# Performance work log

Hardware: AMD Instinct MI355X
Metric: run time of the kernel (lower is better)

Reference implementation:

```python
import jax, jax.numpy as jnp
import numpy as np

B, QLEN, KLEN = 4, 512, 1024
KDIM = QDIM = ADIM = 512
H_MA, H_CA = 4, 2
CHUNK = 4
EPS = 1e-6
SHARP = 1.0
SCALE = float(np.sqrt(ADIM))


def moving_sum(x, back, forward):
    # moving sum over last axis with window [i-back, i+forward] (matches F.conv1d with ones filter)
    nb = [(0, 0)] * (x.ndim - 1)
    cs = jnp.cumsum(jnp.pad(x, nb + [(back, forward)]), axis=-1)
    cs = jnp.pad(cs, nb + [(1, 0)])
    w = back + forward + 1
    return cs[..., w:] - cs[..., :-w]


def setup_inputs() -> dict:
    key = jax.random.key(0)
    ks = jax.random.split(key, 16)
    s = 0.02
    f32 = jnp.float32
    return {
        'key_t': jax.random.normal(ks[0], (B, KLEN, KDIM), f32),
        'query': jax.random.normal(ks[1], (B, QLEN, QDIM), f32),
        # monotonic energy params
        'wk_ma': jax.random.normal(ks[2], (KDIM, ADIM), f32) * s,
        'bk_ma': jnp.zeros((ADIM,), f32),
        'wq_ma': jax.random.normal(ks[3], (QDIM, ADIM), f32) * s,
        'bq_ma': jnp.zeros((ADIM,), f32),
        'r': jnp.array([-4.0], f32),
        # chunk energy params
        'wk_ca': jax.random.normal(ks[4], (KDIM, ADIM), f32) * s,
        'bk_ca': jnp.zeros((ADIM,), f32),
        'wq_ca': jax.random.normal(ks[5], (QDIM, ADIM), f32) * s,
        'bq_ca': jnp.zeros((ADIM,), f32),
        # value / output projections
        'wv': jax.random.normal(ks[6], (KDIM, ADIM), f32) * s,
        'bv': jnp.zeros((ADIM,), f32),
        'wo': jax.random.normal(ks[7], (ADIM, ADIM), f32) * s,
        'bo': jnp.zeros((ADIM,), f32),
    }


def reference(key_t, query, wk_ma, bk_ma, wq_ma, bq_ma, r,
              wk_ca, bk_ca, wq_ca, bq_ca, wv, bv, wo, bo):
    # ---- monotonic energy (scaled_dot) -> [B, H_ma, qlen, klen]
    dk = ADIM // H_MA
    k_ma = (key_t @ wk_ma + bk_ma).reshape(B, KLEN, H_MA, dk).transpose(0, 2, 1, 3)
    q_ma = (query @ wq_ma + bq_ma).reshape(B, QLEN, H_MA, dk).transpose(0, 2, 1, 3)
    e_ma = jnp.einsum('bhqd,bhkd->bhqk', q_ma, k_ma) / SCALE + r[0]

    # ---- selection probabilities + safe cumprod of (1 - p) (exclusive, in log space)
    p = jax.nn.sigmoid(e_ma)                              # [B,H,q,k]
    log1mp = jnp.log(jnp.clip(1.0 - p, EPS, 1.0))
    cp = jnp.exp(jnp.cumsum(log1mp, axis=-1) - log1mp)    # exclusive cumprod

    # ---- monotonic alignment alpha via recurrence over query steps (parallel MoChA)
    aw0 = jnp.zeros((B, H_MA, KLEN), p.dtype).at[:, :, 0].set(1.0)

    def step(aw_prev, pc):
        p_i, cp_i = pc  # [B,H,k]
        a = p_i * cp_i * jnp.cumsum(aw_prev / jnp.clip(cp_i, EPS, 1.0), axis=-1)
        return a, a

    _, alpha_q = jax.lax.scan(step, aw0, (jnp.moveaxis(p, 2, 0), jnp.moveaxis(cp, 2, 0)))
    alpha = jnp.moveaxis(alpha_q, 0, 2)                   # [B,H_ma,q,k]

    # ---- chunk energy (scaled_dot, shared across MA heads) -> [B, H_ca, qlen, klen]
    dkc = ADIM // H_CA
    k_ca = (key_t @ wk_ca + bk_ca).reshape(B, KLEN, H_CA, dkc).transpose(0, 2, 1, 3)
    q_ca = (query @ wq_ca + bq_ca).reshape(B, QLEN, H_CA, dkc).transpose(0, 2, 1, 3)
    e_ca = jnp.einsum('bhqd,bhkd->bhqk', q_ca, k_ca) / SCALE

    # ---- efficient chunkwise attention: clipped-exp softmax within moving window
    u = e_ca - jnp.max(e_ca, axis=-1, keepdims=True)
    se = jnp.maximum(jnp.exp(u), 1e-5)                    # [B,H_ca,q,k]
    denom = moving_sum(se, CHUNK - 1, 0)                  # [B,H_ca,q,k]
    frac = alpha[:, :, None] * SHARP / denom[:, None]     # [B,H_ma,H_ca,q,k]
    beta = se[:, None] * moving_sum(frac, 0, CHUNK - 1)   # [B,H_ma,H_ca,q,k]
    beta = beta.reshape(B, H_MA * H_CA, QLEN, KLEN)

    # ---- context vector and output projection
    h = H_MA * H_CA
    dv = ADIM // h
    v = (key_t @ wv + bv).reshape(B, KLEN, h, dv).transpose(0, 2, 1, 3)
    cv = jnp.einsum('bhqk,bhkd->bhqd', beta, v)
    cv = cv.transpose(0, 2, 1, 3).reshape(B, QLEN, ADIM)
    return cv @ wo + bo
```

## Files before the change

kernel.cpp:

```cpp
#include <hip/hip_runtime.h>
#include <hip/hip_bf16.h>
#include <math.h>

#define DEV_INLINE __device__ __forceinline__

typedef float f32x4 __attribute__((ext_vector_type(4)));
typedef short bf16x8 __attribute__((ext_vector_type(8)));
typedef short s16x4 __attribute__((ext_vector_type(4)));

constexpr int B_    = 4;
constexpr int QLEN  = 512;
constexpr int KLEN  = 1024;
constexpr int DIM   = 512;
constexpr int H_MA  = 4;
constexpr int H_CA  = 2;
constexpr int CHUNK = 4;
constexpr float EPS = 1e-6f;
constexpr float INV_SCALE = 1.0f / 22.62741699796952f;


DEV_INLINE unsigned short f2bf(float x) {
    unsigned int u = __float_as_uint(x);
    unsigned int r = u + 0x7FFFu + ((u >> 16) & 1u);
    return (unsigned short)(r >> 16);
}

DEV_INLINE void split2(float x, short& h, short& l) {
    const unsigned short hb = f2bf(x);
    const float hf = __uint_as_float(((unsigned int)hb) << 16);
    h = (short)hb;
    l = (short)f2bf(x - hf);
}

DEV_INLINE float bf2f(short s) {
    return __uint_as_float(((unsigned int)(unsigned short)s) << 16);
}

__global__ __launch_bounds__(256) void rowsplit2_kernel(
    const float* __restrict__ X0, short* __restrict__ H0, short* __restrict__ L0, int n0_4,
    const float* __restrict__ X1, short* __restrict__ H1, short* __restrict__ L1, int n1_4)
{
    int i = blockIdx.x * 256 + threadIdx.x;
    const float* X; short* Xh; short* Xl;
    if (i < n0_4) { X = X0; Xh = H0; Xl = L0; }
    else {
        i -= n0_4;
        if (i >= n1_4) return;
        X = X1; Xh = H1; Xl = L1;
    }
    const f32x4 v = *(const f32x4*)(X + (size_t)i * 4);
    s16x4 h, l;
#pragma unroll
    for (int j = 0; j < 4; ++j) {
        short hh, ll;
        split2(v[j], hh, ll);
        h[j] = hh; l[j] = ll;
    }
    *(s16x4*)(Xh + (size_t)i * 4) = h;
    *(s16x4*)(Xl + (size_t)i * 4) = l;
}

__global__ __launch_bounds__(256) void transsplit6_kernel(
    const float* __restrict__ w0, const float* __restrict__ w1,
    const float* __restrict__ w2, const float* __restrict__ w3,
    const float* __restrict__ w4, const float* __restrict__ w5,
    short* __restrict__ WTkh, short* __restrict__ WTkl,
    short* __restrict__ WTqh, short* __restrict__ WTql,
    short* __restrict__ WToh, short* __restrict__ WTol)
{
    const float* W; short* Dh; short* Dl;
    const int zz = blockIdx.z;
    const int MS = 512 * 512;
    switch (zz) {
        case 0: W = w0; Dh = WTkh;          Dl = WTkl;          break;
        case 1: W = w1; Dh = WTkh + MS;     Dl = WTkl + MS;     break;
        case 2: W = w2; Dh = WTkh + 2 * MS; Dl = WTkl + 2 * MS; break;
        case 3: W = w3; Dh = WTqh;          Dl = WTql;          break;
        case 4: W = w4; Dh = WTqh + MS;     Dl = WTql + MS;     break;
        default: W = w5; Dh = WToh;         Dl = WTol;          break;
    }

    __shared__ __align__(16) short Th[64][72];
    __shared__ __align__(16) short Tl[64][72];
    const int t = threadIdx.x;
    const int k0 = blockIdx.x * 64;
    const int n0 = blockIdx.y * 64;
#pragma unroll
    for (int i = 0; i < 4; ++i) {
        const int c  = t + 256 * i;
        const int kr = c >> 4;
        const int nc = c & 15;
        const f32x4 v = *(const f32x4*)(W + (size_t)(k0 + kr) * DIM + n0 + nc * 4);
#pragma unroll
        for (int j = 0; j < 4; ++j) {
            short h, l;
            split2(v[j], h, l);
            Th[nc * 4 + j][kr] = h;
            Tl[nc * 4 + j][kr] = l;
        }
    }
    __syncthreads();
#pragma unroll
    for (int i = 0; i < 4; ++i) {
        const int c  = t + 256 * i;
        const int nr = c >> 4;
        const int kc = c & 15;
        *(s16x4*)(Dh + (size_t)(n0 + nr) * DIM + k0 + kc * 4) = *(const s16x4*)&Th[nr][kc * 4];
        *(s16x4*)(Dl + (size_t)(n0 + nr) * DIM + k0 + kc * 4) = *(const s16x4*)&Tl[nr][kc * 4];
    }
}


DEV_INLINE void mfma128_nt_core(
    const short* __restrict__ Ah, const short* __restrict__ Al, int lda,
    const short* __restrict__ Bh, const short* __restrict__ Bl, int ldb,
    int K, int bm, int bn, f32x4 (&acc)[4][4])
{
    __shared__ __align__(16) short AsH[8][4][16][8];
    __shared__ __align__(16) short AsL[8][4][16][8];
    __shared__ __align__(16) short BsH[8][4][16][8];
    __shared__ __align__(16) short BsL[8][4][16][8];
    const int tid  = threadIdx.x;
    const int lane = tid & 63;
    const int w    = tid >> 6;
    const int wm   = w >> 1, wn = w & 1;
    const int lkg  = lane >> 4, lrow = lane & 15;

    for (int k0 = 0; k0 < K; k0 += 32) {
        bf16x8 vah[2], val[2], vbh[2], vbl[2];
#pragma unroll
        for (int p = 0; p < 2; ++p) {
            const int c = p * 256 + tid;
            const int row = c >> 2, kk = c & 3;
            const size_t ao = (size_t)(bm + row) * lda + k0 + kk * 8;
            const size_t bo = (size_t)(bn + row) * ldb + k0 + kk * 8;
            vah[p] = *(const bf16x8*)(Ah + ao);
            val[p] = *(const bf16x8*)(Al + ao);
            vbh[p] = *(const bf16x8*)(Bh + bo);
            vbl[p] = *(const bf16x8*)(Bl + bo);
        }
        __syncthreads();
#pragma unroll
        for (int p = 0; p < 2; ++p) {
            const int c = p * 256 + tid;
            const int row = c >> 2, kk = c & 3;
            const int fm = row >> 4, rr = row & 15;
            *(bf16x8*)&AsH[fm][kk][rr][0] = vah[p];
            *(bf16x8*)&AsL[fm][kk][rr][0] = val[p];
            *(bf16x8*)&BsH[fm][kk][rr][0] = vbh[p];
            *(bf16x8*)&BsL[fm][kk][rr][0] = vbl[p];
        }
        __syncthreads();

        bf16x8 bhf[4], blf[4];
#pragma unroll
        for (int fn = 0; fn < 4; ++fn) {
            bhf[fn] = *(const bf16x8*)&BsH[wn * 4 + fn][lkg][lrow][0];
            blf[fn] = *(const bf16x8*)&BsL[wn * 4 + fn][lkg][lrow][0];
        }
#pragma unroll
        for (int fm = 0; fm < 4; ++fm) {
            const bf16x8 ah = *(const bf16x8*)&AsH[wm * 4 + fm][lkg][lrow][0];
            const bf16x8 al = *(const bf16x8*)&AsL[wm * 4 + fm][lkg][lrow][0];
#pragma unroll
            for (int fn = 0; fn < 4; ++fn) {
                acc[fm][fn] = __builtin_amdgcn_mfma_f32_16x16x32_bf16(ah, bhf[fn], acc[fm][fn], 0, 0, 0);
                acc[fm][fn] = __builtin_amdgcn_mfma_f32_16x16x32_bf16(ah, blf[fn], acc[fm][fn], 0, 0, 0);
                acc[fm][fn] = __builtin_amdgcn_mfma_f32_16x16x32_bf16(al, bhf[fn], acc[fm][fn], 0, 0, 0);
            }
        }
    }
}

__global__ __launch_bounds__(256) void proj_both_kernel(
    const short* __restrict__ Kh, const short* __restrict__ Kl,
    const short* __restrict__ Qh, const short* __restrict__ Ql,
    const short* __restrict__ WTkh, const short* __restrict__ WTkl,
    const short* __restrict__ WTqh, const short* __restrict__ WTql,
    short* __restrict__ KPh, short* __restrict__ KPl,
    short* __restrict__ QPh, short* __restrict__ QPl,
    const float* __restrict__ bkma, const float* __restrict__ bkca,
    const float* __restrict__ bvv_,
    const float* __restrict__ bqma, const float* __restrict__ bqca)
{
    const int bid = blockIdx.x;
    const short *Ah, *Al, *Bh, *Bl;
    short *Ch, *Cl;
    const float *b0, *b1, *b2;
    int bm, bn, ldc;
    if (bid < 384) {
        bm = (bid & 31) * 128; bn = (bid >> 5) * 128;
        Ah = Kh; Al = Kl; Bh = WTkh; Bl = WTkl;
        Ch = KPh; Cl = KPl; ldc = 1536;
        b0 = bkma; b1 = bkca; b2 = bvv_;
    } else {
        const int r = bid - 384;
        bm = (r & 15) * 128; bn = (r >> 4) * 128;
        Ah = Qh; Al = Ql; Bh = WTqh; Bl = WTql;
        Ch = QPh; Cl = QPl; ldc = 1024;
        b0 = bqma; b1 = bqca; b2 = bqca;
    }

    f32x4 acc[4][4] = {};
    mfma128_nt_core(Ah, Al, DIM, Bh, Bl, DIM, DIM, bm, bn, acc);
    const int lane = threadIdx.x & 63;
    const int w = threadIdx.x >> 6;
    const int wm = w >> 1, wn = w & 1;
#pragma unroll
    for (int fm = 0; fm < 4; ++fm)
#pragma unroll
        for (int fn = 0; fn < 4; ++fn) {
            const int col = bn + wn * 64 + fn * 16 + (lane & 15);
            const int seg = col >> 9, cs = col & 511;
            const float bvv = seg == 0 ? b0[cs] : (seg == 1 ? b1[cs] : b2[cs]);
#pragma unroll
            for (int j = 0; j < 4; ++j) {
                const int row = bm + wm * 64 + fm * 16 + (lane >> 4) * 4 + j;
                short h, l;
                split2(acc[fm][fn][j] + bvv, h, l);
                Ch[(size_t)row * ldc + col] = h;
                Cl[(size_t)row * ldc + col] = l;
            }
        }
}

__global__ __launch_bounds__(256) void energy_both_kernel(
    const short* __restrict__ QPh, const short* __restrict__ QPl,
    const short* __restrict__ KPh, const short* __restrict__ KPl,
    float* __restrict__ EMA, float* __restrict__ ECA,
    const float* __restrict__ radd)
{
    const int gz = blockIdx.z;
    int colA0, colB0, HD;
    float* E;
    float addv;
    int b, h;
    if (gz < 16) {
        b = gz >> 2; h = gz & 3;
        colA0 = 0; colB0 = 0; HD = 128;
        E = EMA + (size_t)gz * QLEN * KLEN;
        addv = radd[0];
    } else {
        const int z = gz - 16;
        b = z >> 1; h = z & 1;
        colA0 = 512; colB0 = 512; HD = 256;
        E = ECA + (size_t)z * QLEN * KLEN;
        addv = 0.0f;
    }
    const short* Ah = QPh + (size_t)b * QLEN * 1024 + colA0 + h * HD;
    const short* Al = QPl + (size_t)b * QLEN * 1024 + colA0 + h * HD;
    const short* Bh = KPh + (size_t)b * KLEN * 1536 + colB0 + h * HD;
    const short* Bl = KPl + (size_t)b * KLEN * 1536 + colB0 + h * HD;

    f32x4 acc[4][4] = {};
    const int bm = blockIdx.x * 128, bn = blockIdx.y * 128;
    mfma128_nt_core(Ah, Al, 1024, Bh, Bl, 1536, HD, bm, bn, acc);
    const int lane = threadIdx.x & 63;
    const int w = threadIdx.x >> 6;
    const int wm = w >> 1, wn = w & 1;
#pragma unroll
    for (int fm = 0; fm < 4; ++fm)
#pragma unroll
        for (int fn = 0; fn < 4; ++fn) {
            const int col = bn + wn * 64 + fn * 16 + (lane & 15);
#pragma unroll
            for (int j = 0; j < 4; ++j) {
                const int row = bm + wm * 64 + fm * 16 + (lane >> 4) * 4 + j;
                E[(size_t)row * KLEN + col] = acc[fm][fn][j] * INV_SCALE + addv;
            }
        }
}


DEV_INLINE void mfma_nt_core(const short* __restrict__ Ah, const short* __restrict__ Al, int lda,
                             const short* __restrict__ Bh, const short* __restrict__ Bl, int ldb,
                             int K, int bm, int bn, f32x4 (&acc)[2][2])
{
    __shared__ __align__(16) short AsH[4][4][16][8];
    __shared__ __align__(16) short AsL[4][4][16][8];
    __shared__ __align__(16) short BsH[4][4][16][8];
    __shared__ __align__(16) short BsL[4][4][16][8];
    const int tid  = threadIdx.x;
    const int lane = tid & 63;
    const int w    = tid >> 6;
    const int wm   = w >> 1, wn = w & 1;
    const int r    = tid >> 2;
    const int kg   = tid & 3;
    const int rb   = r >> 4, rr = r & 15;
    const int lkg  = lane >> 4, lrr = lane & 15;

    for (int k0 = 0; k0 < K; k0 += 32) {
        const bf16x8 avh = *(const bf16x8*)(Ah + (size_t)(bm + r) * lda + k0 + kg * 8);
        const bf16x8 avl = *(const bf16x8*)(Al + (size_t)(bm + r) * lda + k0 + kg * 8);
        const bf16x8 bvh = *(const bf16x8*)(Bh + (size_t)(bn + r) * ldb + k0 + kg * 8);
        const bf16x8 bvl = *(const bf16x8*)(Bl + (size_t)(bn + r) * ldb + k0 + kg * 8);
        __syncthreads();
        *(bf16x8*)&AsH[rb][kg][rr][0] = avh;
        *(bf16x8*)&AsL[rb][kg][rr][0] = avl;
        *(bf16x8*)&BsH[rb][kg][rr][0] = bvh;
        *(bf16x8*)&BsL[rb][kg][rr][0] = bvl;
        __syncthreads();
#pragma unroll
        for (int fm = 0; fm < 2; ++fm) {
            const bf16x8 ah = *(const bf16x8*)&AsH[wm * 2 + fm][lkg][lrr][0];
            const bf16x8 al = *(const bf16x8*)&AsL[wm * 2 + fm][lkg][lrr][0];
#pragma unroll
            for (int fn = 0; fn < 2; ++fn) {
                const bf16x8 bh = *(const bf16x8*)&BsH[wn * 2 + fn][lkg][lrr][0];
                const bf16x8 bl = *(const bf16x8*)&BsL[wn * 2 + fn][lkg][lrr][0];
                acc[fm][fn] = __builtin_amdgcn_mfma_f32_16x16x32_bf16(ah, bh, acc[fm][fn], 0, 0, 0);
                acc[fm][fn] = __builtin_amdgcn_mfma_f32_16x16x32_bf16(ah, bl, acc[fm][fn], 0, 0, 0);
                acc[fm][fn] = __builtin_amdgcn_mfma_f32_16x16x32_bf16(al, bh, acc[fm][fn], 0, 0, 0);
            }
        }
    }
}

__global__ __launch_bounds__(256) void mfma_nt_f32_kernel(
    const short* __restrict__ Ah, const short* __restrict__ Al, int lda,
    const short* __restrict__ Bh, const short* __restrict__ Bl, int ldb,
    float* __restrict__ C, int ldc, int K,
    const float* __restrict__ bias)
{
    f32x4 acc[2][2] = {};
    const int bm = blockIdx.x * 64, bn = blockIdx.y * 64;
    mfma_nt_core(Ah, Al, lda, Bh, Bl, ldb, K, bm, bn, acc);
    const int lane = threadIdx.x & 63;
    const int w = threadIdx.x >> 6;
    const int wm = w >> 1, wn = w & 1;
#pragma unroll
    for (int fm = 0; fm < 2; ++fm)
#pragma unroll
        for (int fn = 0; fn < 2; ++fn) {
            const int col = bn + wn * 32 + fn * 16 + (lane & 15);
            const float bvv = bias ? bias[col] : 0.0f;
#pragma unroll
            for (int j = 0; j < 4; ++j) {
                const int row = bm + wm * 32 + fm * 16 + (lane >> 4) * 4 + j;
                C[(size_t)row * ldc + col] = acc[fm][fn][j] + bvv;
            }
        }
}


__global__ __launch_bounds__(256) void rows_kernel(
    float* __restrict__ PCP, float* __restrict__ ICP,
    float* __restrict__ SE, float* __restrict__ RDEN)
{
    const int bid = blockIdx.x;
    const int tid = threadIdx.x;
    const int lane = tid & 63, wid = tid >> 6;

    if (bid < B_ * H_MA * QLEN) {
        const size_t row = bid;
        float* pe = PCP + row * KLEN;
        float* pi = ICP + row * KLEN;

        const float4 ev = *(const float4*)(pe + tid * 4);
        float e[4] = {ev.x, ev.y, ev.z, ev.w};
        float p[4], l[4], s[4];
        float run = 0.0f;
#pragma unroll
        for (int j = 0; j < 4; ++j) {
            p[j] = 1.0f / (1.0f + expf(-e[j]));
            float om = 1.0f - p[j];
            om = fminf(fmaxf(om, EPS), 1.0f);
            l[j] = logf(om);
            run += l[j];
            s[j] = run;
        }
        const float t = run;
        float v = t;
#pragma unroll
        for (int off = 1; off < 64; off <<= 1) {
            const float u = __shfl_up(v, off);
            if (lane >= off) v += u;
        }
        __shared__ float wsum[4];
        if (lane == 63) wsum[wid] = v;
        __syncthreads();
        float base = v - t;
        for (int w = 0; w < wid; ++w) base += wsum[w];

        float4 po, io;
        float* pp = (float*)&po;
        float* ip = (float*)&io;
#pragma unroll
        for (int j = 0; j < 4; ++j) {
            const float cum = base + s[j];
            const float cp  = expf(cum - l[j]);
            pp[j] = p[j] * cp;
            ip[j] = 1.0f / fmaxf(cp, EPS);
        }
        *(float4*)(pe + tid * 4) = po;
        *(float4*)(pi + tid * 4) = io;
    } else {
        const size_t row = bid - B_ * H_MA * QLEN;
        float* ps = SE + row * KLEN;
        float* pd = RDEN + row * KLEN;

        const float4 ev = *(const float4*)(ps + tid * 4);
        float e[4] = {ev.x, ev.y, ev.z, ev.w};
        float m = fmaxf(fmaxf(e[0], e[1]), fmaxf(e[2], e[3]));
#pragma unroll
        for (int off = 32; off >= 1; off >>= 1)
            m = fmaxf(m, __shfl_xor(m, off));
        __shared__ float wmax[4];
        if (lane == 0) wmax[wid] = m;
        __syncthreads();
        m = fmaxf(fmaxf(wmax[0], wmax[1]), fmaxf(wmax[2], wmax[3]));

        __shared__ float sh[KLEN + 3];
        if (tid < 3) sh[tid] = 0.0f;
        float se[4];
#pragma unroll
        for (int j = 0; j < 4; ++j) {
            se[j] = fmaxf(expf(e[j] - m), 1e-5f);
            sh[3 + tid * 4 + j] = se[j];
        }
        __syncthreads();
        float4 so, do_;
        float* sp = (float*)&so;
        float* dp = (float*)&do_;
#pragma unroll
        for (int j = 0; j < 4; ++j) {
            const int k = tid * 4 + j;
            sp[j] = se[j];
            dp[j] = 1.0f / (sh[3 + k] + sh[2 + k] + sh[1 + k] + sh[k]);
        }
        *(float4*)(ps + tid * 4) = so;
        *(float4*)(pd + tid * 4) = do_;
    }
}


template<int CTRL, int ROW_MASK>
DEV_INLINE float dpp_add(float x) {
    int t = __builtin_amdgcn_update_dpp(0, __float_as_int(x), CTRL, ROW_MASK, 0xf, true);
    return x + __int_as_float(t);
}

DEV_INLINE float wave64_incl_scan(float x) {
    x = dpp_add<0x111, 0xf>(x);
    x = dpp_add<0x112, 0xf>(x);
    x = dpp_add<0x114, 0xf>(x);
    x = dpp_add<0x118, 0xf>(x);
    x = dpp_add<0x142, 0xa>(x);
    x = dpp_add<0x143, 0xc>(x);
    return x;
}

typedef __attribute__((address_space(3))) void lv_t;
typedef __attribute__((address_space(1))) const void gv_t;

DEV_INLINE void dma16(const float* g, float* l) {
    __builtin_amdgcn_global_load_lds((gv_t*)g, (lv_t*)l, 16, 0, 0);
}

template<int N> DEV_INLINE void vwait() {
    asm volatile("s_waitcnt vmcnt(%0)" :: "i"(N) : "memory");
    __builtin_amdgcn_sched_barrier(0);
}

template<int N> DEV_INLINE void lwait() {
    asm volatile("s_waitcnt lgkmcnt(%0)" :: "i"(N));
    __builtin_amdgcn_sched_barrier(0);
}

DEV_INLINE void ldsr4(f32x4& d, const float* a_) {
    const unsigned off = (unsigned)(size_t)(lv_t*)a_;
    asm volatile("ds_read_b128 %0, %1" : "=v"(d) : "v"(off));
}

DEV_INLINE void dswr1(float* a_, float v) {
    const unsigned off = (unsigned)(size_t)(lv_t*)a_;
    asm volatile("ds_write_b32 %0, %1" :: "v"(off), "v"(v));
}

DEV_INLINE void sbar() {
    asm volatile("s_barrier" ::: "memory");
}

#define ASTEP(WAITN, BUF, NBUF, PAR, DO_READ, DO_DMA, CG, NG)         \
    {                                                                 \
        vwait<WAITN>();                                               \
        if (DO_READ) {                                                \
            ldsr4(p##NG, &ring[NBUF][0][qoff]);                       \
            ldsr4(i##NG, &ring[NBUF][1][qoff]);                       \
        }                                                             \
        const float t0 = a0 * i##CG[0];                               \
        const float t1 = a1 * i##CG[1];                               \
        const float t2 = a2 * i##CG[2];                               \
        const float t3 = a3 * i##CG[3];                               \
        const float s1 = t0 + t1;                                     \
        const float s2 = s1 + t2;                                     \
        const float s3 = s2 + t3;                                     \
        const float incl = wave64_incl_scan(s3);                      \
        const float excl = incl - s3;                                 \
        if (lane == 63) dswr1(&tot[PAR][wq], incl);                   \
        lwait<0>();                                                   \
        sbar();                                                       \
        f32x4 T;                                                      \
        ldsr4(T, &tot[PAR][0]);                                       \
        lwait<0>();                                                   \
        float Tpre = excl;                                            \
        if (wq > 0) Tpre += T[0];                                     \
        if (wq > 1) Tpre += T[1];                                     \
        if (wq > 2) Tpre += T[2];                                     \
        a0 = p##CG[0] * (Tpre + t0);                                  \
        a1 = p##CG[1] * (Tpre + s1);                                  \
        a2 = p##CG[2] * (Tpre + s2);                                  \
        a3 = p##CG[3] * (Tpre + s3);                                  \
        f32x4 av = {a0, a1, a2, a3};                                  \
        *(f32x4*)st = av;                                             \
        st += KLEN;                                                   \
        __builtin_amdgcn_sched_barrier(0);                            \
        if (DO_DMA) {                                                 \
            dma16(np, &ring[BUF][0][wq * 256]);                       \
            dma16(ni, &ring[BUF][1][wq * 256]);                       \
            np += KLEN; ni += KLEN;                                   \
        }                                                             \
    }

__global__ __launch_bounds__(256) void alpha_kernel(
    const float* __restrict__ PCPin, const float* __restrict__ ICP,
    float* __restrict__ AOUT)
{
    __shared__ __align__(16) float ring[8][2][1024];
    __shared__ __align__(16) float tot[2][4];

    const int z = blockIdx.x;
    const float* base = PCPin + (size_t)z * QLEN * KLEN;
    const float* ibase = ICP + (size_t)z * QLEN * KLEN;
    float* obase = AOUT + (size_t)z * QLEN * KLEN;
    const int tid  = threadIdx.x;
    const int lane = tid & 63;
    const int wq   = tid >> 6;
    const int qoff = wq * 256 + lane * 4;

    {
        const float* pp = base + qoff;
        const float* ip = ibase + qoff;
#pragma unroll
        for (int rr = 0; rr < 8; ++rr) {
            dma16(pp, &ring[rr][0][wq * 256]);
            dma16(ip, &ring[rr][1][wq * 256]);
            pp += KLEN; ip += KLEN;
        }
    }

    f32x4 pA, iA, pB, iB;
    vwait<14>();
    ldsr4(pA, &ring[0][0][qoff]);
    ldsr4(iA, &ring[0][1][qoff]);
    lwait<0>();

    float a0 = 0.0f, a1 = 0.0f, a2 = 0.0f, a3 = 0.0f;
    if (qoff == 0) a0 = 1.0f;

    float* st = obase + qoff;
    const float* np = base + (size_t)8 * KLEN + qoff;
    const float* ni = ibase + (size_t)8 * KLEN + qoff;

    for (int it = 0; it < 63; ++it) {
        ASTEP(12, 0, 1, 0, true, true, A, B)
        ASTEP(12, 1, 2, 1, true, true, B, A)
        ASTEP(12, 2, 3, 0, true, true, A, B)
        ASTEP(12, 3, 4, 1, true, true, B, A)
        ASTEP(12, 4, 5, 0, true, true, A, B)
        ASTEP(12, 5, 6, 1, true, true, B, A)
        ASTEP(12, 6, 7, 0, true, true, A, B)
        ASTEP(12, 7, 0, 1, true, true, B, A)
    }

    ASTEP(12, 0, 1, 0, true, false, A, B)
    ASTEP(10, 1, 2, 1, true, false, B, A)
    ASTEP(8,  2, 3, 0, true, false, A, B)
    ASTEP(6,  3, 4, 1, true, false, B, A)
    ASTEP(4,  4, 5, 0, true, false, A, B)
    ASTEP(2,  5, 6, 1, true, false, B, A)
    ASTEP(0,  6, 7, 0, true, false, A, B)
    ASTEP(0,  7, 0, 1, false, false, B, A)
}


__global__ __launch_bounds__(256) void fused_cv_mfma_kernel(
    const float* __restrict__ ALPHA, const float* __restrict__ SE,
    const float* __restrict__ RDEN,
    const short* __restrict__ VPh, const short* __restrict__ VPl, int ldv,
    short* __restrict__ CVh, short* __restrict__ CVl)
{
    const int z = blockIdx.y;
    const int b = z >> 3;
    const int h = z & 7;
    const int hma = h >> 1;
    const int hca = h & 1;
    const int bm = blockIdx.x * 64;

    const float* a_base  = ALPHA + ((size_t)b * H_MA + hma) * QLEN * KLEN;
    const float* se_base = SE   + ((size_t)b * H_CA + hca) * QLEN * KLEN;
    const float* dn_base = RDEN + ((size_t)b * H_CA + hca) * QLEN * KLEN;
    const short* vh_base = VPh + (size_t)b * KLEN * ldv + 1024 + h * 64;
    const short* vl_base = VPl + (size_t)b * KLEN * ldv + 1024 + h * 64;
    short* Ch = CVh + (size_t)b * QLEN * DIM + h * 64;
    short* Cl = CVl + (size_t)b * QLEN * DIM + h * 64;

    __shared__ __align__(16) short AsH[4][4][16][8];
    __shared__ __align__(16) short AsL[4][4][16][8];
    __shared__ __align__(16) short BsH[4][4][16][8];
    __shared__ __align__(16) short BsL[4][4][16][8];

    const int tid  = threadIdx.x;
    const int lane = tid & 63;
    const int w    = tid >> 6;
    const int wm   = w >> 1, wn = w & 1;
    const int lkg  = lane >> 4, lrr = lane & 15;
    const int arow = tid >> 2;
    const int aoct = tid & 3;
    const int vk  = tid >> 3;
    const int vn8 = (tid & 7) * 8;

    f32x4 acc[2][2] = {};

    for (int k0 = 0; k0 < KLEN; k0 += 32) {
        const int ka = k0 + aoct * 8;
        const size_t roff = (size_t)(bm + arow) * KLEN;
        const f32x4 se0 = *(const f32x4*)(se_base + roff + ka);
        const f32x4 se1 = *(const f32x4*)(se_base + roff + ka + 4);
        const f32x4 al0 = *(const f32x4*)(a_base + roff + ka);
        const f32x4 al1 = *(const f32x4*)(a_base + roff + ka + 4);
        const f32x4 dn0 = *(const f32x4*)(dn_base + roff + ka);
        const f32x4 dn1 = *(const f32x4*)(dn_base + roff + ka + 4);
        f32x4 al2 = {0.0f, 0.0f, 0.0f, 0.0f};
        f32x4 dn2 = {1.0f, 1.0f, 1.0f, 1.0f};
        if (ka + 8 < KLEN) {
            al2 = *(const f32x4*)(a_base + roff + ka + 8);
            dn2 = *(const f32x4*)(dn_base + roff + ka + 8);
        }
        float ad[11];
#pragma unroll
        for (int j = 0; j < 4; ++j) ad[j] = al0[j] * dn0[j];
#pragma unroll
        for (int j = 0; j < 4; ++j) ad[4 + j] = al1[j] * dn1[j];
#pragma unroll
        for (int j = 0; j < 3; ++j) ad[8 + j] = al2[j] * dn2[j];
        bf16x8 bh_, bl_;
#pragma unroll
        for (int j = 0; j < 8; ++j) {
            const float sej = j < 4 ? se0[j] : se1[j - 4];
            const float beta = sej * (ad[j] + ad[j + 1] + ad[j + 2] + ad[j + 3]);
            short hh, ll;
            split2(beta, hh, ll);
            bh_[j] = hh; bl_[j] = ll;
        }
        const bf16x8 vvh = *(const bf16x8*)(vh_base + (size_t)(k0 + vk) * ldv + vn8);
        const bf16x8 vvl = *(const bf16x8*)(vl_base + (size_t)(k0 + vk) * ldv + vn8);
        __syncthreads();
        *(bf16x8*)&AsH[arow >> 4][aoct][arow & 15][0] = bh_;
        *(bf16x8*)&AsL[arow >> 4][aoct][arow & 15][0] = bl_;
#pragma unroll
        for (int j = 0; j < 8; ++j) {
            const int n = vn8 + j;
            BsH[n >> 4][vk >> 3][n & 15][vk & 7] = vvh[j];
            BsL[n >> 4][vk >> 3][n & 15][vk & 7] = vvl[j];
        }
        __syncthreads();
#pragma unroll
        for (int fm = 0; fm < 2; ++fm) {
            const bf16x8 ah = *(const bf16x8*)&AsH[wm * 2 + fm][lkg][lrr][0];
            const bf16x8 al = *(const bf16x8*)&AsL[wm * 2 + fm][lkg][lrr][0];
#pragma unroll
            for (int fn = 0; fn < 2; ++fn) {
                const bf16x8 vh = *(const bf16x8*)&BsH[wn * 2 + fn][lkg][lrr][0];
                const bf16x8 vl = *(const bf16x8*)&BsL[wn * 2 + fn][lkg][lrr][0];
                acc[fm][fn] = __builtin_amdgcn_mfma_f32_16x16x32_bf16(ah, vh, acc[fm][fn], 0, 0, 0);
                acc[fm][fn] = __builtin_amdgcn_mfma_f32_16x16x32_bf16(ah, vl, acc[fm][fn], 0, 0, 0);
                acc[fm][fn] = __builtin_amdgcn_mfma_f32_16x16x32_bf16(al, vh, acc[fm][fn], 0, 0, 0);
            }
        }
    }

#pragma unroll
    for (int fm = 0; fm < 2; ++fm)
#pragma unroll
        for (int fn = 0; fn < 2; ++fn) {
            const int col = wn * 32 + fn * 16 + (lane & 15);
#pragma unroll
            for (int j = 0; j < 4; ++j) {
                const int row = bm + wm * 32 + fm * 16 + (lane >> 4) * 4 + j;
                short hh, ll;
                split2(acc[fm][fn][j], hh, ll);
                const size_t ro = (size_t)row * DIM + col;
                Ch[ro] = hh;
                Cl[ro] = ll;
            }
        }
}


extern "C" void kernel_launch(void* const* d_in, const int* in_sizes, int n_in,
                              void* d_out, int out_size, void* d_ws, size_t ws_size,
                              hipStream_t stream)
{
    (void)in_sizes; (void)n_in; (void)out_size; (void)ws_size;
    const float* key_t = (const float*)d_in[0];
    const float* query = (const float*)d_in[1];
    const float* wk_ma = (const float*)d_in[2];
    const float* bk_ma = (const float*)d_in[3];
    const float* wq_ma = (const float*)d_in[4];
    const float* bq_ma = (const float*)d_in[5];
    const float* r     = (const float*)d_in[6];
    const float* wk_ca = (const float*)d_in[7];
    const float* bk_ca = (const float*)d_in[8];
    const float* wq_ca = (const float*)d_in[9];
    const float* bq_ca = (const float*)d_in[10];
    const float* wv    = (const float*)d_in[11];
    const float* bv    = (const float*)d_in[12];
    const float* wo    = (const float*)d_in[13];
    const float* bo    = (const float*)d_in[14];
    float* out = (float*)d_out;

    char* w8 = (char*)d_ws;
    size_t off = 0;
    auto take = [&](size_t n) { char* p = w8 + off; off += n; return p; };
    float* PCP = (float*)take(32ull << 20);
    float* ICP = (float*)take(32ull << 20);
    float* SE  = (float*)take(16ull << 20);
    float* DEN = (float*)take(16ull << 20);
    char* keyrg = take(8ull << 20);
    short* keyh = (short*)keyrg;
    short* keyl = (short*)(keyrg + (4ull << 20));
    short* CVh  = (short*)keyrg;
    short* CVl  = (short*)(keyrg + (2ull << 20));
    short* qh = (short*)take(2ull << 20);
    short* ql = (short*)take(2ull << 20);
    short* WTkh = (short*)take((size_t)1536 * 512 * 2);
    short* WTkl = (short*)take((size_t)1536 * 512 * 2);
    short* WTqh = (short*)take((size_t)1024 * 512 * 2);
    short* WTql = (short*)take((size_t)1024 * 512 * 2);
    short* WToh = (short*)take((size_t)512 * 512 * 2);
    short* WTol = (short*)take((size_t)512 * 512 * 2);
    short* KPh = (short*)take((size_t)4096 * 1536 * 2);
    short* KPl = (short*)take((size_t)4096 * 1536 * 2);
    short* QPh = (short*)take((size_t)2048 * 1024 * 2);
    short* QPl = (short*)take((size_t)2048 * 1024 * 2);

    const dim3 blk(256);
    const int KEL4 = B_ * KLEN * DIM / 4;
    const int QEL4 = B_ * QLEN * DIM / 4;

    rowsplit2_kernel<<<dim3((KEL4 + QEL4 + 255) / 256), blk, 0, stream>>>(
        key_t, keyh, keyl, KEL4, query, qh, ql, QEL4);
    transsplit6_kernel<<<dim3(8, 8, 6), blk, 0, stream>>>(
        wk_ma, wk_ca, wv, wq_ma, wq_ca, wo,
        WTkh, WTkl, WTqh, WTql, WToh, WTol);

    proj_both_kernel<<<dim3(512), blk, 0, stream>>>(
        keyh, keyl, qh, ql, WTkh, WTkl, WTqh, WTql,
        KPh, KPl, QPh, QPl, bk_ma, bk_ca, bv, bq_ma, bq_ca);

    energy_both_kernel<<<dim3(QLEN / 128, KLEN / 128, 24), blk, 0, stream>>>(
        QPh, QPl, KPh, KPl, PCP, SE, r);

    rows_kernel<<<dim3(B_ * H_MA * QLEN + B_ * H_CA * QLEN), blk, 0, stream>>>(
        PCP, ICP, SE, DEN);

    alpha_kernel<<<dim3(B_ * H_MA), blk, 0, stream>>>(PCP, ICP, PCP);

    fused_cv_mfma_kernel<<<dim3(QLEN / 64, B_ * H_MA * H_CA), blk, 0, stream>>>(
        PCP, SE, DEN, KPh, KPl, 1536, CVh, CVl);

    mfma_nt_f32_kernel<<<dim3(B_ * QLEN / 64, DIM / 64), blk, 0, stream>>>(
        CVh, CVl, DIM, WToh, WTol, DIM, out, DIM, DIM, bo);
}
```

Before: 296.7 us.

## Make alpha scan wave-redundant to remove per-row cross-wave barrier

Each of the four waves now computes the whole 1024-column row scan itself, with 16 elements per lane and a single wave64 scan. This removes the per-row LDS exchange of partial totals and the barrier between waves. The LDS ring grows to 16 slots and is refilled in batches of 8 rows, with one barrier per batch instead of one per row. In exchange every wave does the scan arithmetic four times and only one wave stores each 16-column slice, so the loop depends on batched prefetch keeping the serial dependency chain fed.

```diff
diff --git a/kernel.cpp b/kernel.cpp
--- a/kernel.cpp
+++ b/kernel.cpp
@@ -472,115 +472,127 @@
     asm volatile("ds_read_b128 %0, %1" : "=v"(d) : "v"(off));
 }
 
-DEV_INLINE void dswr1(float* a_, float v) {
-    const unsigned off = (unsigned)(size_t)(lv_t*)a_;
-    asm volatile("ds_write_b32 %0, %1" :: "v"(off), "v"(v));
-}
-
 DEV_INLINE void sbar() {
     asm volatile("s_barrier" ::: "memory");
 }
 
-#define ASTEP(WAITN, BUF, NBUF, PAR, DO_READ, DO_DMA, CG, NG)         \
-    {                                                                 \
-        vwait<WAITN>();                                               \
-        if (DO_READ) {                                                \
-            ldsr4(p##NG, &ring[NBUF][0][qoff]);                       \
-            ldsr4(i##NG, &ring[NBUF][1][qoff]);                       \
-        }                                                             \
-        const float t0 = a0 * i##CG[0];                               \
-        const float t1 = a1 * i##CG[1];                               \
-        const float t2 = a2 * i##CG[2];                               \
-        const float t3 = a3 * i##CG[3];                               \
-        const float s1 = t0 + t1;                                     \
-        const float s2 = s1 + t2;                                     \
-        const float s3 = s2 + t3;                                     \
-        const float incl = wave64_incl_scan(s3);                      \
-        const float excl = incl - s3;                                 \
-        if (lane == 63) dswr1(&tot[PAR][wq], incl);                   \
-        lwait<0>();                                                   \
-        sbar();                                                       \
-        f32x4 T;                                                      \
-        ldsr4(T, &tot[PAR][0]);                                       \
-        lwait<0>();                                                   \
-        float Tpre = excl;                                            \
-        if (wq > 0) Tpre += T[0];                                     \
-        if (wq > 1) Tpre += T[1];                                     \
-        if (wq > 2) Tpre += T[2];                                     \
-        a0 = p##CG[0] * (Tpre + t0);                                  \
-        a1 = p##CG[1] * (Tpre + s1);                                  \
-        a2 = p##CG[2] * (Tpre + s2);                                  \
-        a3 = p##CG[3] * (Tpre + s3);                                  \
-        f32x4 av = {a0, a1, a2, a3};                                  \
-        *(f32x4*)st = av;                                             \
-        st += KLEN;                                                   \
-        __builtin_amdgcn_sched_barrier(0);                            \
-        if (DO_DMA) {                                                 \
-            dma16(np, &ring[BUF][0][wq * 256]);                       \
-            dma16(ni, &ring[BUF][1][wq * 256]);                       \
-            np += KLEN; ni += KLEN;                                   \
-        }                                                             \
+DEV_INLINE void alpha_step(const f32x4& P0, const f32x4& P1,
+                           const f32x4& P2, const f32x4& P3,
+                           const f32x4& I0, const f32x4& I1,
+                           const f32x4& I2, const f32x4& I3,
+                           float (&a)[16])
+{
+    float pc[16], ic[16];
+    *(f32x4*)&pc[0] = P0; *(f32x4*)&pc[4] = P1;
+    *(f32x4*)&pc[8] = P2; *(f32x4*)&pc[12] = P3;
+    *(f32x4*)&ic[0] = I0; *(f32x4*)&ic[4] = I1;
+    *(f32x4*)&ic[8] = I2; *(f32x4*)&ic[12] = I3;
+
+    float t[16];
+#pragma unroll
+    for (int j = 0; j < 16; ++j) t[j] = a[j] * ic[j];
+
+    float u1[8], u2[4];
+#pragma unroll
+    for (int j = 0; j < 8; ++j) u1[j] = t[2 * j] + t[2 * j + 1];
+#pragma unroll
+    for (int j = 0; j < 4; ++j) u2[j] = u1[2 * j] + u1[2 * j + 1];
+    const float tot = (u2[0] + u2[1]) + (u2[2] + u2[3]);
+
+    const float incl = wave64_incl_scan(tot);
+    const float excl = incl - tot;
+
+    float s = 0.0f;
+#pragma unroll
+    for (int j = 0; j < 16; ++j) {
+        s += t[j];
+        a[j] = pc[j] * (excl + s);
+    }
+}
+
+#define RD(slot, G)                                       \
+    ldsr4(p##G##0, &ring[slot][0][0   + 4 * lane]);       \
+    ldsr4(p##G##1, &ring[slot][0][256 + 4 * lane]);       \
+    ldsr4(p##G##2, &ring[slot][0][512 + 4 * lane]);       \
+    ldsr4(p##G##3, &ring[slot][0][768 + 4 * lane]);       \
+    ldsr4(i##G##0, &ring[slot][1][0   + 4 * lane]);       \
+    ldsr4(i##G##1, &ring[slot][1][256 + 4 * lane]);       \
+    ldsr4(i##G##2, &ring[slot][1][512 + 4 * lane]);       \
+    ldsr4(i##G##3, &ring[slot][1][768 + 4 * lane]);
+
+#define ALSTEP(G)                                                     \
+    alpha_step(p##G##0, p##G##1, p##G##2, p##G##3,                    \
+               i##G##0, i##G##1, i##G##2, i##G##3, a);
+
+#define STQ(r)                                                        \
+    if ((lane >> 4) == wq) {                                          \
+        float* st = obase + (size_t)(r) * KLEN + col;                 \
+        *(f32x4*)(st + 0)  = *(const f32x4*)&a[0];                    \
+        *(f32x4*)(st + 4)  = *(const f32x4*)&a[4];                    \
+        *(f32x4*)(st + 8)  = *(const f32x4*)&a[8];                    \
+        *(f32x4*)(st + 12) = *(const f32x4*)&a[12];                   \
     }
 
 __global__ __launch_bounds__(256) void alpha_kernel(
     const float* __restrict__ PCPin, const float* __restrict__ ICP,
     float* __restrict__ AOUT)
 {
-    __shared__ __align__(16) float ring[8][2][1024];
-    __shared__ __align__(16) float tot[2][4];
+    __shared__ __align__(16) float ring[16][2][1024];
 
     const int z = blockIdx.x;
-    const float* base = PCPin + (size_t)z * QLEN * KLEN;
-    const float* ibase = ICP + (size_t)z * QLEN * KLEN;
+    const float* base  = PCPin + (size_t)z * QLEN * KLEN;
+    const float* ibase = ICP   + (size_t)z * QLEN * KLEN;
     float* obase = AOUT + (size_t)z * QLEN * KLEN;
     const int tid  = threadIdx.x;
     const int lane = tid & 63;
     const int wq   = tid >> 6;
-    const int qoff = wq * 256 + lane * 4;
+    const int col  = lane * 16;
 
     {
-        const float* pp = base + qoff;
-        const float* ip = ibase + qoff;
+        const float* ps = base  + col + 4 * wq;
+        const float* is = ibase + col + 4 * wq;
 #pragma unroll
         for (int rr = 0; rr < 8; ++rr) {
-            dma16(pp, &ring[rr][0][wq * 256]);
-            dma16(ip, &ring[rr][1][wq * 256]);
-            pp += KLEN; ip += KLEN;
-        }
-    }
-
-    f32x4 pA, iA, pB, iB;
-    vwait<14>();
-    ldsr4(pA, &ring[0][0][qoff]);
-    ldsr4(iA, &ring[0][1][qoff]);
-    lwait<0>();
-
-    float a0 = 0.0f, a1 = 0.0f, a2 = 0.0f, a3 = 0.0f;
-    if (qoff == 0) a0 = 1.0f;
-
-    float* st = obase + qoff;
-    const float* np = base + (size_t)8 * KLEN + qoff;
-    const float* ni = ibase + (size_t)8 * KLEN + qoff;
-
-    for (int it = 0; it < 63; ++it) {
-        ASTEP(12, 0, 1, 0, true, true, A, B)
-        ASTEP(12, 1, 2, 1, true, true, B, A)
-        ASTEP(12, 2, 3, 0, true, true, A, B)
-        ASTEP(12, 3, 4, 1, true, true, B, A)
-        ASTEP(12, 4, 5, 0, true, true, A, B)
-        ASTEP(12, 5, 6, 1, true, true, B, A)
-        ASTEP(12, 6, 7, 0, true, true, A, B)
-        ASTEP(12, 7, 0, 1, true, true, B, A)
-    }
-
-    ASTEP(12, 0, 1, 0, true, false, A, B)
-    ASTEP(10, 1, 2, 1, true, false, B, A)
-    ASTEP(8,  2, 3, 0, true, false, A, B)
-    ASTEP(6,  3, 4, 1, true, false, B, A)
-    ASTEP(4,  4, 5, 0, true, false, A, B)
-    ASTEP(2,  5, 6, 1, true, false, B, A)
-    ASTEP(0,  6, 7, 0, true, false, A, B)
-    ASTEP(0,  7, 0, 1, false, false, B, A)
+            dma16(ps, &ring[rr][0][wq * 256]);
+            dma16(is, &ring[rr][1][wq * 256]);
+            ps += KLEN; is += KLEN;
+        }
+    }
+    vwait<0>();
+    sbar();
+
+    float a[16];
+#pragma unroll
+    for (int j = 0; j < 16; ++j) a[j] = 0.0f;
+    if (lane == 0) a[0] = 1.0f;
+
+    f32x4 pA0, pA1, pA2, pA3, iA0, iA1, iA2, iA3;
+    f32x4 pB0, pB1, pB2, pB3, iB0, iB1, iB2, iB3;
+
+    for (int w = 0; w < 64; ++w) {
+        const int R = w * 8;
+        if (w < 63) {
+            const float* ps = base  + (size_t)(R + 8) * KLEN + col + 4 * wq;
+            const float* is = ibase + (size_t)(R + 8) * KLEN + col + 4 * wq;
+#pragma unroll
+            for (int rr = 0; rr < 8; ++rr) {
+                dma16(ps, &ring[(R + 8 + rr) & 15][0][wq * 256]);
+                dma16(is, &ring[(R + 8 + rr) & 15][1][wq * 256]);
+                ps += KLEN; is += KLEN;
+            }
+        }
+        RD((R + 0) & 15, A)
+        RD((R + 1) & 15, B)  lwait<8>();  ALSTEP(A)  STQ(R + 0)
+        RD((R + 2) & 15, A)  lwait<8>();  ALSTEP(B)  STQ(R + 1)
+        RD((R + 3) & 15, B)  lwait<8>();  ALSTEP(A)  STQ(R + 2)
+        RD((R + 4) & 15, A)  lwait<8>();  ALSTEP(B)  STQ(R + 3)
+        RD((R + 5) & 15, B)  lwait<8>();  ALSTEP(A)  STQ(R + 4)
+        RD((R + 6) & 15, A)  lwait<8>();  ALSTEP(B)  STQ(R + 5)
+        RD((R + 7) & 15, B)  lwait<8>();  ALSTEP(A)  STQ(R + 6)
+                             lwait<0>();  ALSTEP(B)  STQ(R + 7)
+        vwait<0>();
+        sbar();
+    }
 }
 
 
```

After: 374.9 us. 1.26x slower.
